# Kernel tuning notes

Hardware: AMD Instinct MI355X
Metric: run time of the kernel (lower is better)

## Reference

```python
import jax, jax.numpy as jnp
import numpy as np

ALPHA = 1.702
LIMIT = 7.0
EPS = 1e-5
TOP_K = 4


def setup_inputs() -> dict:
    key = jax.random.key(0)
    ks = jax.random.split(key, 8)
    B, S, H, I, E = 2, 512, 2048, 2048, 16
    return {
        "x": jax.random.normal(ks[0], (B, S, H), jnp.float32),
        "norm_w": jnp.ones((H,), jnp.float32),
        "gate_w": jax.random.normal(ks[1], (E, H), jnp.float32) * 0.02,
        "gate_b": jax.random.normal(ks[2], (E,), jnp.float32) * 0.02,
        "w1": jax.random.normal(ks[3], (E, 2 * I, H), jnp.float32) * 0.02,
        "b1": jax.random.normal(ks[4], (E, 2 * I), jnp.float32) * 0.02,
        "w2": jax.random.normal(ks[5], (E, H, I), jnp.float32) * 0.02,
        "b2": jax.random.normal(ks[6], (E, H), jnp.float32) * 0.02,
    }


def reference(x, norm_w, gate_w, gate_b, w1, b1, w2, b2):
    B, S, H = x.shape
    M = B * S
    E = gate_w.shape[0]
    xf = x.reshape(M, H)
    # RMSNorm
    t = xf * jax.lax.rsqrt(jnp.mean(xf * xf, axis=-1, keepdims=True) + EPS) * norm_w
    # Router: top-k over logits, then softmax over the selected k (sm_first=False)
    logits = t @ gate_w.T + gate_b  # [M, E]
    vals, idx = jax.lax.top_k(logits, TOP_K)
    gates_k = jax.nn.softmax(vals, axis=-1)  # [M, k]
    # Scatter top-k gate weights into dense [M, E] combine matrix
    G = jnp.zeros((M, E), x.dtype).at[jnp.arange(M)[:, None], idx].set(gates_k)
    # Expert MLP1 (all experts, combined sparsely below): [E, M, 2I]
    h = jnp.einsum('mh,eoh->emo', t, w1) + b1[:, None, :]
    # SwiGLU with clamp (gpt-oss): interleaved gate/linear columns
    a = jnp.minimum(h[..., ::2], LIMIT)
    b = jnp.clip(h[..., 1::2], -LIMIT, LIMIT)
    act = a * jax.nn.sigmoid(ALPHA * a) * (b + 1.0)  # [E, M, I]
    # Expert MLP2: [E, M, H]
    y = jnp.einsum('emi,edi->emd', act, w2) + b2[:, None, :]
    # Combine with gate weights (gammas scale full per-expert output incl. bias)
    delta = jnp.einsum('me,emd->md', G, y)
    return x + delta.reshape(B, S, H)
```

## Files before the change

kernel.cpp:

```cpp
#include <hip/hip_runtime.h>
#include <hip/hip_bf16.h>

constexpr int MTOK = 1024;
constexpr int HDIM = 2048;
constexpr int IDIM = 2048;
constexpr int NEXP = 16;
constexpr int TOPK = 4;
constexpr int NA   = MTOK * TOPK;

#define ALPHA_C 1.702f
#define LIMIT_C 7.0f
#define RMS_EPS 1e-5f

using short8   = __attribute__((ext_vector_type(8))) short;
using f32x4    = __attribute__((ext_vector_type(4))) float;

__device__ __forceinline__ unsigned short f2bf(float f) {
    unsigned u = __builtin_bit_cast(unsigned, f);
    u += 0x7fffu + ((u >> 16) & 1u);
    return (unsigned short)(u >> 16);
}

__device__ __forceinline__ unsigned pack2bf(float lo, float hi) {
    return (unsigned)f2bf(lo) | ((unsigned)f2bf(hi) << 16);
}

__device__ __forceinline__ short8 cvt8(const float4 a, const float4 b) {
    union { short8 s; unsigned u[4]; } r;
    r.u[0] = pack2bf(a.x, a.y);
    r.u[1] = pack2bf(a.z, a.w);
    r.u[2] = pack2bf(b.x, b.y);
    r.u[3] = pack2bf(b.z, b.w);
    return r.s;
}

__global__ void k_copy(const float* __restrict__ x, float* __restrict__ out, int n4) {
    int i = blockIdx.x * blockDim.x + threadIdx.x;
    int stride = gridDim.x * blockDim.x;
    const float4* xs = (const float4*)x;
    float4* os = (float4*)out;
    for (; i < n4; i += stride) os[i] = xs[i];
}

__global__ __launch_bounds__(256) void k_router(
    const float* __restrict__ x, const float* __restrict__ norm_w,
    const float* __restrict__ gate_w, const float* __restrict__ gate_b,
    unsigned short* __restrict__ t_bf,
    int* __restrict__ counts, int* __restrict__ idx_of,
    int* __restrict__ slot_of, float* __restrict__ gate_mk)
{
    __shared__ float t_lds[HDIM];
    __shared__ float red[4];
    __shared__ float logits[NEXP];

    const int m   = blockIdx.x;
    const int tid = threadIdx.x;
    const float* xr = x + (size_t)m * HDIM;

    float4 v0 = ((const float4*)xr)[tid * 2];
    float4 v1 = ((const float4*)xr)[tid * 2 + 1];
    float ss = v0.x*v0.x + v0.y*v0.y + v0.z*v0.z + v0.w*v0.w
             + v1.x*v1.x + v1.y*v1.y + v1.z*v1.z + v1.w*v1.w;
    #pragma unroll
    for (int off = 32; off > 0; off >>= 1) ss += __shfl_down(ss, off);
    if ((tid & 63) == 0) red[tid >> 6] = ss;
    __syncthreads();
    float tot = red[0] + red[1] + red[2] + red[3];
    float scale = rsqrtf(tot / (float)HDIM + RMS_EPS);

    float4 n0 = ((const float4*)norm_w)[tid * 2];
    float4 n1 = ((const float4*)norm_w)[tid * 2 + 1];
    float t[8];
    t[0]=v0.x*scale*n0.x; t[1]=v0.y*scale*n0.y; t[2]=v0.z*scale*n0.z; t[3]=v0.w*scale*n0.w;
    t[4]=v1.x*scale*n1.x; t[5]=v1.y*scale*n1.y; t[6]=v1.z*scale*n1.z; t[7]=v1.w*scale*n1.w;
    short8 pk;
    #pragma unroll
    for (int j = 0; j < 8; ++j) {
        t_lds[tid * 8 + j] = t[j];
        pk[j] = (short)f2bf(t[j]);
    }
    *(short8*)(t_bf + (size_t)m * HDIM + tid * 8) = pk;
    __syncthreads();

    const int e = tid >> 4, j = tid & 15;
    const float* gw = gate_w + (size_t)e * HDIM;
    float part = 0.f;
    for (int h = j; h < HDIM; h += 16) part += t_lds[h] * gw[h];
    #pragma unroll
    for (int off = 8; off > 0; off >>= 1) part += __shfl_xor(part, off);
    if (j == 0) logits[e] = part + gate_b[e];
    __syncthreads();

    if (tid == 0) {
        float lv[NEXP];
        #pragma unroll
        for (int q = 0; q < NEXP; ++q) lv[q] = logits[q];
        int   sel[TOPK];
        float sv[TOPK];
        #pragma unroll
        for (int k = 0; k < TOPK; ++k) {
            float best = -1e30f; int bi = 0;
            for (int q = 0; q < NEXP; ++q)
                if (lv[q] > best) { best = lv[q]; bi = q; }
            sel[k] = bi; sv[k] = best; lv[bi] = -1e30f;
        }
        float mx = sv[0], s = 0.f, g[TOPK];
        #pragma unroll
        for (int k = 0; k < TOPK; ++k) { g[k] = __expf(sv[k] - mx); s += g[k]; }
        float inv = 1.f / s;
        #pragma unroll
        for (int k = 0; k < TOPK; ++k) {
            int a = m * TOPK + k;
            int slot = atomicAdd(&counts[sel[k]], 1);
            idx_of[a]  = sel[k];
            slot_of[a] = slot;
            gate_mk[a] = g[k] * inv;
        }
    }
}

__global__ void k_offsets(const int* __restrict__ counts, int* __restrict__ offsets) {
    if (threadIdx.x == 0) {
        int s = 0;
        for (int e = 0; e < NEXP; ++e) { offsets[e] = s; s += counts[e]; }
        offsets[NEXP] = s;
    }
}

__global__ void k_remap(const int* __restrict__ idx_of, const int* __restrict__ slot_of,
                        const float* __restrict__ gate_mk, const int* __restrict__ offsets,
                        int* __restrict__ token_of, float* __restrict__ gate_row)
{
    int a = blockIdx.x * blockDim.x + threadIdx.x;
    if (a >= NA) return;
    int e = idx_of[a];
    int r = offsets[e] + slot_of[a];
    token_of[r] = a >> 2;
    gate_row[r] = gate_mk[a];
}

__global__ __launch_bounds__(256) void k_gemm1(
    const unsigned short* __restrict__ t_bf,
    const float* __restrict__ w1, const float* __restrict__ b1,
    const int* __restrict__ counts, const int* __restrict__ offsets,
    const int* __restrict__ token_of,
    unsigned short* __restrict__ act)
{
    __shared__ unsigned char lA[2][20480];
    __shared__ unsigned char lB[2][5120];

    const int e  = blockIdx.z;
    const int ne = counts[e];
    const int brow = blockIdx.y * 320;
    if (brow >= ne) return;
    const int roff = offsets[e];
    const int i0 = blockIdx.x * 32;
    const int tid = threadIdx.x;

    const int wv = tid >> 6, ln = tid & 63;
    const int lr = ln & 15, lk = ln >> 4;
    const int ar = tid >> 2, ap = tid & 3;

    const unsigned short* asrc[5];
    #pragma unroll
    for (int it = 0; it < 5; ++it) {
        int rr = brow + ar + it * 64;
        int tok = token_of[roff + (rr < ne ? rr : 0)];
        asrc[it] = t_bf + (size_t)tok * HDIM + ap * 8;
    }
    const int o = (ar < 32) ? (2 * (i0 + ar)) : (2 * (i0 + ar - 32) + 1);
    const float* bsrc = w1 + ((size_t)e * (2 * IDIM) + o) * HDIM + ap * 8;

    short8 aR[5];
    float4 bR0, bR1;

    f32x4 acc[5][4] = {};

    #pragma unroll
    for (int it = 0; it < 5; ++it) aR[it] = *(const short8*)(asrc[it]);
    bR0 = *(const float4*)(bsrc);
    bR1 = *(const float4*)(bsrc + 4);
    #pragma unroll
    for (int it = 0; it < 5; ++it)
        *(short8*)(&lA[0][(ap * 320 + ar + it * 64) * 16]) = aR[it];
    *(short8*)(&lB[0][ar * 80 + ap * 16]) = cvt8(bR0, bR1);
    #pragma unroll
    for (int it = 0; it < 5; ++it) aR[it] = *(const short8*)(asrc[it] + 32);
    bR0 = *(const float4*)(bsrc + 32);
    bR1 = *(const float4*)(bsrc + 32 + 4);
    asm volatile("s_waitcnt lgkmcnt(0)" ::: "memory");
    __builtin_amdgcn_s_barrier();

    for (int t = 0; t < 64; ++t) {
        const int c = t & 1;
        if (t + 1 < 64) {
            #pragma unroll
            for (int it = 0; it < 5; ++it)
                *(short8*)(&lA[c ^ 1][(ap * 320 + ar + it * 64) * 16]) = aR[it];
            *(short8*)(&lB[c ^ 1][ar * 80 + ap * 16]) = cvt8(bR0, bR1);
        }
        if (t + 2 < 64) {
            #pragma unroll
            for (int it = 0; it < 5; ++it)
                aR[it] = *(const short8*)(asrc[it] + (t + 2) * 32);
            bR0 = *(const float4*)(bsrc + (t + 2) * 32);
            bR1 = *(const float4*)(bsrc + (t + 2) * 32 + 4);
        }
        short8 afr[5], bfr[4];
        #pragma unroll
        for (int mf = 0; mf < 5; ++mf)
            afr[mf] = *(const short8*)(&lA[c][(lk * 320 + wv * 80 + mf * 16 + lr) * 16]);
        #pragma unroll
        for (int n = 0; n < 4; ++n)
            bfr[n] = *(const short8*)(&lB[c][(n * 16 + lr) * 80 + lk * 16]);
        #pragma unroll
        for (int mf = 0; mf < 5; ++mf)
            #pragma unroll
            for (int n = 0; n < 4; ++n)
                acc[mf][n] = __builtin_amdgcn_mfma_f32_16x16x32_bf16(afr[mf], bfr[n], acc[mf][n], 0, 0, 0);
        asm volatile("s_waitcnt lgkmcnt(0)" ::: "memory");
        __builtin_amdgcn_s_barrier();
    }

    #pragma unroll
    for (int n = 0; n < 2; ++n) {
        const int i = i0 + n * 16 + lr;
        const float ba = b1[(size_t)e * (2 * IDIM) + 2 * i];
        const float bb = b1[(size_t)e * (2 * IDIM) + 2 * i + 1];
        #pragma unroll
        for (int mf = 0; mf < 5; ++mf) {
            #pragma unroll
            for (int r = 0; r < 4; ++r) {
                const int rg = brow + wv * 80 + mf * 16 + lk * 4 + r;
                if (rg < ne) {
                    float ha = acc[mf][n][r] + ba;
                    float hb = acc[mf][n + 2][r] + bb;
                    float a = fminf(ha, LIMIT_C);
                    float b = fminf(fmaxf(hb, -LIMIT_C), LIMIT_C);
                    float s = 1.f / (1.f + __expf(-ALPHA_C * a));
                    act[(size_t)(roff + rg) * IDIM + i] = f2bf(a * s * (b + 1.f));
                }
            }
        }
    }
}

__global__ __launch_bounds__(256) void k_gemm2(
    const unsigned short* __restrict__ act,
    const float* __restrict__ w2, const float* __restrict__ b2,
    const int* __restrict__ counts, const int* __restrict__ offsets,
    const int* __restrict__ token_of, const float* __restrict__ gate_row,
    float* __restrict__ out)
{
    __shared__ unsigned char lA[2][20480];
    __shared__ unsigned char lB[2][5120];

    const int e  = blockIdx.z;
    const int ne = counts[e];
    const int brow = blockIdx.y * 320;
    if (brow >= ne) return;
    const int roff = offsets[e];
    const int ks = blockIdx.x & 1;
    const int d0 = (blockIdx.x >> 1) * 64;
    const int kbeg = ks * (IDIM / 2);
    const int tid = threadIdx.x;

    const int wv = tid >> 6, ln = tid & 63;
    const int lr = ln & 15, lk = ln >> 4;
    const int ar = tid >> 2, ap = tid & 3;

    const unsigned short* asrc[5];
    #pragma unroll
    for (int it = 0; it < 5; ++it) {
        int rr = brow + ar + it * 64;
        int rc = (rr < ne) ? rr : 0;
        asrc[it] = act + (size_t)(roff + rc) * IDIM + kbeg + ap * 8;
    }
    const float* bsrc = w2 + ((size_t)e * HDIM + d0 + ar) * IDIM + kbeg + ap * 8;

    short8 aR[5];
    float4 bR0, bR1;

    f32x4 acc[5][4] = {};

    #pragma unroll
    for (int it = 0; it < 5; ++it) aR[it] = *(const short8*)(asrc[it]);
    bR0 = *(const float4*)(bsrc);
    bR1 = *(const float4*)(bsrc + 4);
    #pragma unroll
    for (int it = 0; it < 5; ++it)
        *(short8*)(&lA[0][(ap * 320 + ar + it * 64) * 16]) = aR[it];
    *(short8*)(&lB[0][ar * 80 + ap * 16]) = cvt8(bR0, bR1);
    #pragma unroll
    for (int it = 0; it < 5; ++it) aR[it] = *(const short8*)(asrc[it] + 32);
    bR0 = *(const float4*)(bsrc + 32);
    bR1 = *(const float4*)(bsrc + 32 + 4);
    asm volatile("s_waitcnt lgkmcnt(0)" ::: "memory");
    __builtin_amdgcn_s_barrier();

    for (int t = 0; t < 32; ++t) {
        const int c = t & 1;
        if (t + 1 < 32) {
            #pragma unroll
            for (int it = 0; it < 5; ++it)
                *(short8*)(&lA[c ^ 1][(ap * 320 + ar + it * 64) * 16]) = aR[it];
            *(short8*)(&lB[c ^ 1][ar * 80 + ap * 16]) = cvt8(bR0, bR1);
        }
        if (t + 2 < 32) {
            #pragma unroll
            for (int it = 0; it < 5; ++it)
                aR[it] = *(const short8*)(asrc[it] + (t + 2) * 32);
            bR0 = *(const float4*)(bsrc + (t + 2) * 32);
            bR1 = *(const float4*)(bsrc + (t + 2) * 32 + 4);
        }
        short8 afr[5], bfr[4];
        #pragma unroll
        for (int mf = 0; mf < 5; ++mf)
            afr[mf] = *(const short8*)(&lA[c][(lk * 320 + wv * 80 + mf * 16 + lr) * 16]);
        #pragma unroll
        for (int n = 0; n < 4; ++n)
            bfr[n] = *(const short8*)(&lB[c][(n * 16 + lr) * 80 + lk * 16]);
        #pragma unroll
        for (int mf = 0; mf < 5; ++mf)
            #pragma unroll
            for (int n = 0; n < 4; ++n)
                acc[mf][n] = __builtin_amdgcn_mfma_f32_16x16x32_bf16(afr[mf], bfr[n], acc[mf][n], 0, 0, 0);
        asm volatile("s_waitcnt lgkmcnt(0)" ::: "memory");
        __builtin_amdgcn_s_barrier();
    }

    #pragma unroll
    for (int mf = 0; mf < 5; ++mf) {
        #pragma unroll
        for (int r = 0; r < 4; ++r) {
            const int rg = brow + wv * 80 + mf * 16 + lk * 4 + r;
            if (rg >= ne) continue;
            const int tok = token_of[roff + rg];
            const float g = gate_row[roff + rg];
            float* orow = out + (size_t)tok * HDIM;
            #pragma unroll
            for (int n = 0; n < 4; ++n) {
                const int d = d0 + n * 16 + lr;
                float v = g * acc[mf][n][r];
                if (ks == 0) v += g * b2[(size_t)e * HDIM + d];
                atomicAdd(orow + d, v);
            }
        }
    }
}

extern "C" void kernel_launch(void* const* d_in, const int* in_sizes, int n_in,
                              void* d_out, int out_size, void* d_ws, size_t ws_size,
                              hipStream_t stream) {
    const float* x      = (const float*)d_in[0];
    const float* norm_w = (const float*)d_in[1];
    const float* gate_w = (const float*)d_in[2];
    const float* gate_b = (const float*)d_in[3];
    const float* w1     = (const float*)d_in[4];
    const float* b1     = (const float*)d_in[5];
    const float* w2     = (const float*)d_in[6];
    const float* b2     = (const float*)d_in[7];
    float* out = (float*)d_out;

    char* ws = (char*)d_ws;
    size_t off = 0;
    unsigned short* t_bf = (unsigned short*)(ws + off); off += (size_t)MTOK * HDIM * 2;
    unsigned short* actb = (unsigned short*)(ws + off); off += (size_t)NA * IDIM * 2;
    int*   counts   = (int*)(ws + off);   off += 256;
    int*   offsets  = (int*)(ws + off);   off += 256;
    int*   idx_of   = (int*)(ws + off);   off += (size_t)NA * 4;
    int*   slot_of  = (int*)(ws + off);   off += (size_t)NA * 4;
    float* gate_mk  = (float*)(ws + off); off += (size_t)NA * 4;
    int*   token_of = (int*)(ws + off);   off += (size_t)NA * 4;
    float* gate_row = (float*)(ws + off); off += (size_t)NA * 4;

    (void)hipMemsetAsync(counts, 0, 256, stream);
    k_copy<<<1024, 256, 0, stream>>>(x, out, MTOK * HDIM / 4);
    k_router<<<MTOK, 256, 0, stream>>>(x, norm_w, gate_w, gate_b, t_bf,
                                       counts, idx_of, slot_of, gate_mk);
    k_offsets<<<1, 64, 0, stream>>>(counts, offsets);
    k_remap<<<NA / 256, 256, 0, stream>>>(idx_of, slot_of, gate_mk, offsets,
                                          token_of, gate_row);
    k_gemm1<<<dim3(IDIM / 32, (MTOK + 319) / 320, NEXP), 256, 0, stream>>>(
        t_bf, w1, b1, counts, offsets, token_of, actb);
    k_gemm2<<<dim3((HDIM / 64) * 2, (MTOK + 319) / 320, NEXP), 256, 0, stream>>>(
        actb, w2, b2, counts, offsets, token_of, gate_row, out);
}
```

Measured before the change: 464.6 us.

## Load A fragments directly from global into registers, dropping LDS staging for A

Result: slower. 483.7 us (+4.1%).

```diff
diff --git a/kernel.cpp b/kernel.cpp
--- a/kernel.cpp
+++ b/kernel.cpp
@@ -83,9 +83,13 @@
     __syncthreads();
 
     const int e = tid >> 4, j = tid & 15;
-    const float* gw = gate_w + (size_t)e * HDIM;
+    const float4* gw4 = (const float4*)(gate_w + (size_t)e * HDIM);
+    const float4* tl4 = (const float4*)t_lds;
     float part = 0.f;
-    for (int h = j; h < HDIM; h += 16) part += t_lds[h] * gw[h];
+    for (int h4 = j; h4 < HDIM / 4; h4 += 16) {
+        float4 g = gw4[h4], tv = tl4[h4];
+        part += g.x*tv.x + g.y*tv.y + g.z*tv.z + g.w*tv.w;
+    }
     #pragma unroll
     for (int off = 8; off > 0; off >>= 1) part += __shfl_xor(part, off);
     if (j == 0) logits[e] = part + gate_b[e];
@@ -146,7 +150,6 @@
     const int* __restrict__ token_of,
     unsigned short* __restrict__ act)
 {
-    __shared__ unsigned char lA[2][20480];
     __shared__ unsigned char lB[2][5120];
 
     const int e  = blockIdx.z;
@@ -159,67 +162,84 @@
 
     const int wv = tid >> 6, ln = tid & 63;
     const int lr = ln & 15, lk = ln >> 4;
-    const int ar = tid >> 2, ap = tid & 3;
-
-    const unsigned short* asrc[5];
-    #pragma unroll
-    for (int it = 0; it < 5; ++it) {
-        int rr = brow + ar + it * 64;
-        int tok = token_of[roff + (rr < ne ? rr : 0)];
-        asrc[it] = t_bf + (size_t)tok * HDIM + ap * 8;
-    }
-    const int o = (ar < 32) ? (2 * (i0 + ar)) : (2 * (i0 + ar - 32) + 1);
-    const float* bsrc = w1 + ((size_t)e * (2 * IDIM) + o) * HDIM + ap * 8;
-
-    short8 aR[5];
+    const int br = tid >> 2, bp = tid & 3;
+
+    const unsigned short* aptr[5];
+    #pragma unroll
+    for (int mf = 0; mf < 5; ++mf) {
+        int rg = brow + wv * 80 + mf * 16 + lr;
+        int tok = token_of[roff + (rg < ne ? rg : 0)];
+        aptr[mf] = t_bf + (size_t)tok * HDIM + lk * 8;
+    }
+    const int o = (br < 32) ? (2 * (i0 + br)) : (2 * (i0 + br - 32) + 1);
+    const float* bsrc = w1 + ((size_t)e * (2 * IDIM) + o) * HDIM + bp * 8;
+
+    short8 afrE[5], afrO[5];
     float4 bR0, bR1;
-
     f32x4 acc[5][4] = {};
 
     #pragma unroll
-    for (int it = 0; it < 5; ++it) aR[it] = *(const short8*)(asrc[it]);
+    for (int mf = 0; mf < 5; ++mf) afrE[mf] = *(const short8*)(aptr[mf]);
     bR0 = *(const float4*)(bsrc);
     bR1 = *(const float4*)(bsrc + 4);
-    #pragma unroll
-    for (int it = 0; it < 5; ++it)
-        *(short8*)(&lA[0][(ap * 320 + ar + it * 64) * 16]) = aR[it];
-    *(short8*)(&lB[0][ar * 80 + ap * 16]) = cvt8(bR0, bR1);
-    #pragma unroll
-    for (int it = 0; it < 5; ++it) aR[it] = *(const short8*)(asrc[it] + 32);
+    *(short8*)(&lB[0][br * 80 + bp * 16]) = cvt8(bR0, bR1);
+    #pragma unroll
+    for (int mf = 0; mf < 5; ++mf) afrO[mf] = *(const short8*)(aptr[mf] + 32);
     bR0 = *(const float4*)(bsrc + 32);
     bR1 = *(const float4*)(bsrc + 32 + 4);
     asm volatile("s_waitcnt lgkmcnt(0)" ::: "memory");
     __builtin_amdgcn_s_barrier();
 
-    for (int t = 0; t < 64; ++t) {
-        const int c = t & 1;
-        if (t + 1 < 64) {
-            #pragma unroll
-            for (int it = 0; it < 5; ++it)
-                *(short8*)(&lA[c ^ 1][(ap * 320 + ar + it * 64) * 16]) = aR[it];
-            *(short8*)(&lB[c ^ 1][ar * 80 + ap * 16]) = cvt8(bR0, bR1);
-        }
-        if (t + 2 < 64) {
-            #pragma unroll
-            for (int it = 0; it < 5; ++it)
-                aR[it] = *(const short8*)(asrc[it] + (t + 2) * 32);
-            bR0 = *(const float4*)(bsrc + (t + 2) * 32);
-            bR1 = *(const float4*)(bsrc + (t + 2) * 32 + 4);
-        }
-        short8 afr[5], bfr[4];
-        #pragma unroll
-        for (int mf = 0; mf < 5; ++mf)
-            afr[mf] = *(const short8*)(&lA[c][(lk * 320 + wv * 80 + mf * 16 + lr) * 16]);
-        #pragma unroll
-        for (int n = 0; n < 4; ++n)
-            bfr[n] = *(const short8*)(&lB[c][(n * 16 + lr) * 80 + lk * 16]);
-        #pragma unroll
-        for (int mf = 0; mf < 5; ++mf)
+    for (int tp = 0; tp < 32; ++tp) {
+        {
+            const int t = 2 * tp;
+            *(short8*)(&lB[1][br * 80 + bp * 16]) = cvt8(bR0, bR1);
+            if (t + 2 < 64) {
+                bR0 = *(const float4*)(bsrc + (t + 2) * 32);
+                bR1 = *(const float4*)(bsrc + (t + 2) * 32 + 4);
+            }
+            short8 bfr[4];
             #pragma unroll
             for (int n = 0; n < 4; ++n)
-                acc[mf][n] = __builtin_amdgcn_mfma_f32_16x16x32_bf16(afr[mf], bfr[n], acc[mf][n], 0, 0, 0);
-        asm volatile("s_waitcnt lgkmcnt(0)" ::: "memory");
-        __builtin_amdgcn_s_barrier();
+                bfr[n] = *(const short8*)(&lB[0][(n * 16 + lr) * 80 + lk * 16]);
+            #pragma unroll
+            for (int mf = 0; mf < 5; ++mf)
+                #pragma unroll
+                for (int n = 0; n < 4; ++n)
+                    acc[mf][n] = __builtin_amdgcn_mfma_f32_16x16x32_bf16(afrE[mf], bfr[n], acc[mf][n], 0, 0, 0);
+            if (t + 2 < 64) {
+                #pragma unroll
+                for (int mf = 0; mf < 5; ++mf)
+                    afrE[mf] = *(const short8*)(aptr[mf] + (t + 2) * 32);
+            }
+            asm volatile("s_waitcnt lgkmcnt(0)" ::: "memory");
+            __builtin_amdgcn_s_barrier();
+        }
+        {
+            const int t = 2 * tp + 1;
+            if (t + 1 < 64)
+                *(short8*)(&lB[0][br * 80 + bp * 16]) = cvt8(bR0, bR1);
+            if (t + 2 < 64) {
+                bR0 = *(const float4*)(bsrc + (t + 2) * 32);
+                bR1 = *(const float4*)(bsrc + (t + 2) * 32 + 4);
+            }
+            short8 bfr[4];
+            #pragma unroll
+            for (int n = 0; n < 4; ++n)
+                bfr[n] = *(const short8*)(&lB[1][(n * 16 + lr) * 80 + lk * 16]);
+            #pragma unroll
+            for (int mf = 0; mf < 5; ++mf)
+                #pragma unroll
+                for (int n = 0; n < 4; ++n)
+                    acc[mf][n] = __builtin_amdgcn_mfma_f32_16x16x32_bf16(afrO[mf], bfr[n], acc[mf][n], 0, 0, 0);
+            if (t + 2 < 64) {
+                #pragma unroll
+                for (int mf = 0; mf < 5; ++mf)
+                    afrO[mf] = *(const short8*)(aptr[mf] + (t + 2) * 32);
+            }
+            asm volatile("s_waitcnt lgkmcnt(0)" ::: "memory");
+            __builtin_amdgcn_s_barrier();
+        }
     }
 
     #pragma unroll
@@ -252,7 +272,6 @@
     const int* __restrict__ token_of, const float* __restrict__ gate_row,
     float* __restrict__ out)
 {
-    __shared__ unsigned char lA[2][20480];
     __shared__ unsigned char lB[2][5120];
 
     const int e  = blockIdx.z;
@@ -267,66 +286,83 @@
 
     const int wv = tid >> 6, ln = tid & 63;
     const int lr = ln & 15, lk = ln >> 4;
-    const int ar = tid >> 2, ap = tid & 3;
-
-    const unsigned short* asrc[5];
-    #pragma unroll
-    for (int it = 0; it < 5; ++it) {
-        int rr = brow + ar + it * 64;
-        int rc = (rr < ne) ? rr : 0;
-        asrc[it] = act + (size_t)(roff + rc) * IDIM + kbeg + ap * 8;
-    }
-    const float* bsrc = w2 + ((size_t)e * HDIM + d0 + ar) * IDIM + kbeg + ap * 8;
-
-    short8 aR[5];
+    const int br = tid >> 2, bp = tid & 3;
+
+    const unsigned short* aptr[5];
+    #pragma unroll
+    for (int mf = 0; mf < 5; ++mf) {
+        int rg = brow + wv * 80 + mf * 16 + lr;
+        int rc = (rg < ne) ? rg : 0;
+        aptr[mf] = act + (size_t)(roff + rc) * IDIM + kbeg + lk * 8;
+    }
+    const float* bsrc = w2 + ((size_t)e * HDIM + d0 + br) * IDIM + kbeg + bp * 8;
+
+    short8 afrE[5], afrO[5];
     float4 bR0, bR1;
-
     f32x4 acc[5][4] = {};
 
     #pragma unroll
-    for (int it = 0; it < 5; ++it) aR[it] = *(const short8*)(asrc[it]);
+    for (int mf = 0; mf < 5; ++mf) afrE[mf] = *(const short8*)(aptr[mf]);
     bR0 = *(const float4*)(bsrc);
     bR1 = *(const float4*)(bsrc + 4);
-    #pragma unroll
-    for (int it = 0; it < 5; ++it)
-        *(short8*)(&lA[0][(ap * 320 + ar + it * 64) * 16]) = aR[it];
-    *(short8*)(&lB[0][ar * 80 + ap * 16]) = cvt8(bR0, bR1);
-    #pragma unroll
-    for (int it = 0; it < 5; ++it) aR[it] = *(const short8*)(asrc[it] + 32);
+    *(short8*)(&lB[0][br * 80 + bp * 16]) = cvt8(bR0, bR1);
+    #pragma unroll
+    for (int mf = 0; mf < 5; ++mf) afrO[mf] = *(const short8*)(aptr[mf] + 32);
     bR0 = *(const float4*)(bsrc + 32);
     bR1 = *(const float4*)(bsrc + 32 + 4);
     asm volatile("s_waitcnt lgkmcnt(0)" ::: "memory");
     __builtin_amdgcn_s_barrier();
 
-    for (int t = 0; t < 32; ++t) {
-        const int c = t & 1;
-        if (t + 1 < 32) {
-            #pragma unroll
-            for (int it = 0; it < 5; ++it)
-                *(short8*)(&lA[c ^ 1][(ap * 320 + ar + it * 64) * 16]) = aR[it];
-            *(short8*)(&lB[c ^ 1][ar * 80 + ap * 16]) = cvt8(bR0, bR1);
-        }
-        if (t + 2 < 32) {
-            #pragma unroll
-            for (int it = 0; it < 5; ++it)
-                aR[it] = *(const short8*)(asrc[it] + (t + 2) * 32);
-            bR0 = *(const float4*)(bsrc + (t + 2) * 32);
-            bR1 = *(const float4*)(bsrc + (t + 2) * 32 + 4);
-        }
-        short8 afr[5], bfr[4];
-        #pragma unroll
-        for (int mf = 0; mf < 5; ++mf)
-            afr[mf] = *(const short8*)(&lA[c][(lk * 320 + wv * 80 + mf * 16 + lr) * 16]);
-        #pragma unroll
-        for (int n = 0; n < 4; ++n)
-            bfr[n] = *(const short8*)(&lB[c][(n * 16 + lr) * 80 + lk * 16]);
-        #pragma unroll
-        for (int mf = 0; mf < 5; ++mf)
+    for (int tp = 0; tp < 16; ++tp) {
+        {
+            const int t = 2 * tp;
+            *(short8*)(&lB[1][br * 80 + bp * 16]) = cvt8(bR0, bR1);
+            if (t + 2 < 32) {
+                bR0 = *(const float4*)(bsrc + (t + 2) * 32);
+                bR1 = *(const float4*)(bsrc + (t + 2) * 32 + 4);
+            }
+            short8 bfr[4];
             #pragma unroll
             for (int n = 0; n < 4; ++n)
-                acc[mf][n] = __builtin_amdgcn_mfma_f32_16x16x32_bf16(afr[mf], bfr[n], acc[mf][n], 0, 0, 0);
-        asm volatile("s_waitcnt lgkmcnt(0)" ::: "memory");
-        __builtin_amdgcn_s_barrier();
+                bfr[n] = *(const short8*)(&lB[0][(n * 16 + lr) * 80 + lk * 16]);
+            #pragma unroll
+            for (int mf = 0; mf < 5; ++mf)
+                #pragma unroll
+                for (int n = 0; n < 4; ++n)
+                    acc[mf][n] = __builtin_amdgcn_mfma_f32_16x16x32_bf16(afrE[mf], bfr[n], acc[mf][n], 0, 0, 0);
+            if (t + 2 < 32) {
+                #pragma unroll
+                for (int mf = 0; mf < 5; ++mf)
+                    afrE[mf] = *(const short8*)(aptr[mf] + (t + 2) * 32);
+            }
+            asm volatile("s_waitcnt lgkmcnt(0)" ::: "memory");
+            __builtin_amdgcn_s_barrier();
+        }
+        {
+            const int t = 2 * tp + 1;
+            if (t + 1 < 32)
+                *(short8*)(&lB[0][br * 80 + bp * 16]) = cvt8(bR0, bR1);
+            if (t + 2 < 32) {
+                bR0 = *(const float4*)(bsrc + (t + 2) * 32);
+                bR1 = *(const float4*)(bsrc + (t + 2) * 32 + 4);
+            }
+            short8 bfr[4];
+            #pragma unroll
+            for (int n = 0; n < 4; ++n)
+                bfr[n] = *(const short8*)(&lB[1][(n * 16 + lr) * 80 + lk * 16]);
+            #pragma unroll
+            for (int mf = 0; mf < 5; ++mf)
+                #pragma unroll
+                for (int n = 0; n < 4; ++n)
+                    acc[mf][n] = __builtin_amdgcn_mfma_f32_16x16x32_bf16(afrO[mf], bfr[n], acc[mf][n], 0, 0, 0);
+            if (t + 2 < 32) {
+                #pragma unroll
+                for (int mf = 0; mf < 5; ++mf)
+                    afrO[mf] = *(const short8*)(aptr[mf] + (t + 2) * 32);
+            }
+            asm volatile("s_waitcnt lgkmcnt(0)" ::: "memory");
+            __builtin_amdgcn_s_barrier();
+        }
     }
 
     #pragma unroll
```
